# Optimization experiments

Measured on AMD Instinct MI355X. Metric: run time of the kernel, lower is better.

Reference implementation:

```python
import jax, jax.numpy as jnp
import numpy as np

DIM = 1024
INNER = DIM // 2
DSTATE = 8
KSZ = 3
DTRANK = max(INNER // 8, 4)
B, L = 4, 4096


def setup_inputs() -> dict:
    key = jax.random.key(0)
    ks = jax.random.split(key, 8)
    s = 0.02
    x = jax.random.normal(ks[0], (B, L, DIM), dtype=jnp.float32)
    W_in = jax.random.normal(ks[1], (DIM, DIM), dtype=jnp.float32) * s
    Kx = jax.random.normal(ks[2], (INNER, 1, KSZ), dtype=jnp.float32) * 0.1
    Kz = jax.random.normal(ks[3], (INNER, 1, KSZ), dtype=jnp.float32) * 0.1
    W_xproj = jax.random.normal(ks[4], (DTRANK + 2 * DSTATE, INNER), dtype=jnp.float32) * s
    W_dt = jax.random.normal(ks[5], (INNER, DTRANK), dtype=jnp.float32) * s
    # dt bias: inverse_softplus of exp(linspace(log dt_min, log dt_max))
    dt_init = jnp.exp(jnp.linspace(jnp.log(0.02), jnp.log(0.2), INNER))
    b_dt = jnp.log(jnp.expm1(dt_init)).astype(jnp.float32)
    A_log = jnp.log(jnp.tile(jnp.arange(1, DSTATE + 1, dtype=jnp.float32), (INNER, 1)))
    D = jnp.ones((INNER,), dtype=jnp.float32)
    W_out = jax.random.normal(ks[6], (DIM, DIM), dtype=jnp.float32) * s
    return {"x": x, "W_in": W_in, "Kx": Kx, "Kz": Kz, "W_xproj": W_xproj,
            "W_dt": W_dt, "b_dt": b_dt, "A_log": A_log, "D": D, "W_out": W_out}


def _dwconv_silu(u, kern):
    # u: [B,L,C], kern: [C,1,K] depthwise (groups=C), 'same' padding
    c = u.shape[-1]
    v = jnp.transpose(u, (0, 2, 1))  # [B,C,L]
    v = jax.lax.conv_general_dilated(v, kern, (1,), [(KSZ // 2, KSZ // 2)],
                                     dimension_numbers=("NCH", "OIH", "NCH"),
                                     feature_group_count=c)
    return jax.nn.silu(jnp.transpose(v, (0, 2, 1)))


def _forward(x, W_in, Kx, Kz, W_xproj, W_dt, b_dt, A_log, D, W_out):
    h = jnp.einsum("bld,ed->ble", x, W_in)  # Linear(dim,dim), no bias
    xb, zb = jnp.split(h, 2, axis=-1)       # [B,L,INNER] each
    xb = _dwconv_silu(xb, Kx)
    zb = _dwconv_silu(zb, Kz)
    proj = jnp.einsum("blc,oc->blo", xb, W_xproj)
    dt_raw = proj[..., :DTRANK]
    b_raw = proj[..., DTRANK:DTRANK + DSTATE]
    c_raw = proj[..., DTRANK + DSTATE:]
    delta = jnp.clip(jax.nn.softplus(jnp.einsum("blr,cr->blc", dt_raw, W_dt) + b_dt), 1e-4, 1.0)  # [B,L,C]
    b_term = jnp.tanh(b_raw)  # [B,L,N]
    c_term = jnp.tanh(c_raw)  # [B,L,N]
    a = jax.nn.softplus(A_log) + 1e-4  # [C,N]
    decay = jnp.clip(jnp.exp(-delta[..., None] * a), 1e-4, 1.0)        # [B,L,C,N]
    drive = (1.0 - decay) * (b_term[:, :, None, :] * xb[..., None])    # [B,L,C,N]

    def step(state, inp):
        dec_t, drv_t, c_t, x_t = inp  # [B,C,N], [B,C,N], [B,N], [B,C]
        state = dec_t * state + drv_t
        y = jnp.sum(state * c_t[:, None, :], axis=-1) + D * x_t  # [B,C]
        return state, y

    tm = lambda t: jnp.moveaxis(t, 1, 0)  # time-major
    state0 = jnp.zeros((x.shape[0], INNER, DSTATE), dtype=jnp.float32)
    _, ys = jax.lax.scan(step, state0, (tm(decay), tm(drive), tm(c_term), tm(xb)))
    y = jnp.moveaxis(ys, 0, 1)  # [B,L,INNER]
    return jnp.einsum("bld,ed->ble", jnp.concatenate([y, zb], axis=-1), W_out)


def reference(x, W_in, Kx, Kz, W_xproj, W_dt, b_dt, A_log, D, W_out):
    return _forward(x, W_in, Kx, Kz, W_xproj, W_dt, b_dt, A_log, D, W_out)
```

## Files before the change

kernel.cpp:

```cpp
#include <hip/hip_runtime.h>


using bf16x8 = __attribute__((ext_vector_type(8))) short;
using f32x4  = __attribute__((ext_vector_type(4))) float;

__device__ __forceinline__ unsigned short f2bf(float f) {
  unsigned int u = __float_as_uint(f);
  u = u + 0x7fffu + ((u >> 16) & 1u);
  return (unsigned short)(u >> 16);
}

__device__ __forceinline__ float fsoftplus(float x) {
  return (x > 15.f) ? x : __logf(1.f + __expf(x));
}

__device__ __forceinline__ float ftanh(float x) {
  float v = fminf(fmaxf(x, -15.f), 15.f);
  float e = __expf(2.f * v);
  return (e - 1.f) / (e + 1.f);
}

__global__ __launch_bounds__(256) void cvt_bf16_kernel(
    const float* __restrict__ in, unsigned short* __restrict__ out, int n4) {
  int i = blockIdx.x * 256 + threadIdx.x;
  if (i < n4) {
    float4 v = ((const float4*)in)[i];
    ushort4 o;
    o.x = f2bf(v.x); o.y = f2bf(v.y); o.z = f2bf(v.z); o.w = f2bf(v.w);
    ((ushort4*)out)[i] = o;
  }
}

__global__ __launch_bounds__(256) void cvt_wxp_kernel(
    const float* __restrict__ Wx, unsigned short* __restrict__ out) {
  int i = blockIdx.x * 256 + threadIdx.x;
  int row = i >> 9;
  out[i] = (row < 80) ? f2bf(Wx[i]) : (unsigned short)0;
}


__global__ __launch_bounds__(256) void gemm_proj128(
    const unsigned short* __restrict__ A,
    const unsigned short* __restrict__ B,
    unsigned short* __restrict__ dtr, float* __restrict__ bterm,
    float* __restrict__ cterm, int M, int N, int K) {
  __shared__ short As[128 * 32];
  __shared__ short Bs[128 * 32];
  const int m0 = blockIdx.x * 128;
  const int lane = threadIdx.x & 63;
  const int wv = threadIdx.x >> 6;
  const int wm = (wv >> 1) * 64;
  const int wn = (wv & 1) * 64;
  f32x4 acc[4][4] = {};
  const int row_a = wv * 32 + (lane >> 2);
  const int koff = (lane & 3) * 8;
  const unsigned short* gA = A + (size_t)(m0 + row_a) * K + koff;
  const unsigned short* gB = B + (size_t)row_a * K + koff;
  short* lA = &As[(wv * 32) * 32];
  short* lB = &Bs[(wv * 32) * 32];
  const int r = lane & 15;
  const int q = lane >> 4;
  for (int k0 = 0; k0 < K; k0 += 32) {
    __syncthreads();
    __builtin_amdgcn_global_load_lds((const __attribute__((address_space(1))) void*)(const void*)gA,
                                     (__attribute__((address_space(3))) void*)(void*)lA, 16, 0, 0);
    __builtin_amdgcn_global_load_lds((const __attribute__((address_space(1))) void*)(const void*)(gA + 16 * K),
                                     (__attribute__((address_space(3))) void*)(void*)(lA + 16 * 32), 16, 0, 0);
    __builtin_amdgcn_global_load_lds((const __attribute__((address_space(1))) void*)(const void*)gB,
                                     (__attribute__((address_space(3))) void*)(void*)lB, 16, 0, 0);
    __builtin_amdgcn_global_load_lds((const __attribute__((address_space(1))) void*)(const void*)(gB + 16 * K),
                                     (__attribute__((address_space(3))) void*)(void*)(lB + 16 * 32), 16, 0, 0);
    gA += 32; gB += 32;
    __syncthreads();
    bf16x8 av[4], bv[4];
#pragma unroll
    for (int i = 0; i < 4; ++i)
      av[i] = *(const bf16x8*)&As[(wm + i * 16 + r) * 32 + q * 8];
#pragma unroll
    for (int j = 0; j < 4; ++j)
      bv[j] = *(const bf16x8*)&Bs[(wn + j * 16 + r) * 32 + q * 8];
#pragma unroll
    for (int i = 0; i < 4; ++i)
#pragma unroll
      for (int j = 0; j < 4; ++j)
        acc[i][j] = __builtin_amdgcn_mfma_f32_16x16x32_bf16(av[i], bv[j], acc[i][j], 0, 0, 0);
  }
#pragma unroll
  for (int i = 0; i < 4; ++i)
#pragma unroll
    for (int j = 0; j < 4; ++j) {
      const int col = wn + j * 16 + r;
#pragma unroll
      for (int t = 0; t < 4; ++t) {
        const int row = m0 + wm + i * 16 + q * 4 + t;
        float v = acc[i][j][t];
        if (col < 64)      dtr[(size_t)row * 64 + col] = f2bf(v);
        else if (col < 72) bterm[(size_t)row * 8 + (col - 64)] = ftanh(v);
        else if (col < 80) cterm[(size_t)row * 8 + (col - 72)] = ftanh(v);
      }
    }
}

__global__ __launch_bounds__(256) void gemm_dt128(
    const unsigned short* __restrict__ A,
    const unsigned short* __restrict__ B,
    const float* __restrict__ bdt,
    float* __restrict__ C, int M, int N, int K) {
  __shared__ short As[128 * 32];
  __shared__ short Bs[128 * 32];
  const int m0 = blockIdx.x * 128;
  const int n0 = blockIdx.y * 128;
  const int lane = threadIdx.x & 63;
  const int wv = threadIdx.x >> 6;
  const int wm = (wv >> 1) * 64;
  const int wn = (wv & 1) * 64;
  f32x4 acc[4][4] = {};
  const int row_a = wv * 32 + (lane >> 2);
  const int koff = (lane & 3) * 8;
  const unsigned short* gA = A + (size_t)(m0 + row_a) * K + koff;
  const unsigned short* gB = B + (size_t)(n0 + row_a) * K + koff;
  short* lA = &As[(wv * 32) * 32];
  short* lB = &Bs[(wv * 32) * 32];
  const int r = lane & 15;
  const int q = lane >> 4;
  for (int k0 = 0; k0 < K; k0 += 32) {
    __syncthreads();
    __builtin_amdgcn_global_load_lds((const __attribute__((address_space(1))) void*)(const void*)gA,
                                     (__attribute__((address_space(3))) void*)(void*)lA, 16, 0, 0);
    __builtin_amdgcn_global_load_lds((const __attribute__((address_space(1))) void*)(const void*)(gA + 16 * K),
                                     (__attribute__((address_space(3))) void*)(void*)(lA + 16 * 32), 16, 0, 0);
    __builtin_amdgcn_global_load_lds((const __attribute__((address_space(1))) void*)(const void*)gB,
                                     (__attribute__((address_space(3))) void*)(void*)lB, 16, 0, 0);
    __builtin_amdgcn_global_load_lds((const __attribute__((address_space(1))) void*)(const void*)(gB + 16 * K),
                                     (__attribute__((address_space(3))) void*)(void*)(lB + 16 * 32), 16, 0, 0);
    gA += 32; gB += 32;
    __syncthreads();
    bf16x8 av[4], bv[4];
#pragma unroll
    for (int i = 0; i < 4; ++i)
      av[i] = *(const bf16x8*)&As[(wm + i * 16 + r) * 32 + q * 8];
#pragma unroll
    for (int j = 0; j < 4; ++j)
      bv[j] = *(const bf16x8*)&Bs[(wn + j * 16 + r) * 32 + q * 8];
#pragma unroll
    for (int i = 0; i < 4; ++i)
#pragma unroll
      for (int j = 0; j < 4; ++j)
        acc[i][j] = __builtin_amdgcn_mfma_f32_16x16x32_bf16(av[i], bv[j], acc[i][j], 0, 0, 0);
  }
#pragma unroll
  for (int j = 0; j < 4; ++j) {
    const int col = n0 + wn + j * 16 + r;
    const float bb = bdt[col];
#pragma unroll
    for (int i = 0; i < 4; ++i)
#pragma unroll
      for (int t = 0; t < 4; ++t) {
        float v = acc[i][j][t] + bb;
        float delta = fminf(fmaxf(fsoftplus(v), 1e-4f), 1.f);
        C[(size_t)(m0 + wm + i * 16 + q * 4 + t) * N + col] = delta;
      }
  }
}

__device__ __forceinline__ void g256_stage(short* lds, int slot,
    const unsigned short* sp, int ktIdx, int wvLds, int K) {
  const unsigned short* s = sp + ktIdx * 64;
  __builtin_amdgcn_global_load_lds((const __attribute__((address_space(1))) void*)s,
      (__attribute__((address_space(3))) void*)(lds + slot * 8192 + wvLds), 16, 0, 0);
  __builtin_amdgcn_global_load_lds((const __attribute__((address_space(1))) void*)(s + (size_t)64 * K),
      (__attribute__((address_space(3))) void*)(lds + slot * 8192 + 4096 + wvLds), 16, 0, 0);
}

template <int MP, int MH, int NL, int SSLOT, bool VM, int RK, int RP>
__device__ __forceinline__ void g256_phase(
    short* lds, int aSlotOff, int bSlotOff, int aoff, int boff, int wvLds,
    bf16x8 (&av)[4][2], bf16x8 (&bv)[4][2], f32x4 (&acc)[8][4],
    const unsigned short* sp, int ktIdx, int K) {
  g256_stage(lds, SSLOT, sp, ktIdx, wvLds, K);
  if (VM) asm volatile("s_waitcnt vmcnt(6)" ::: "memory");
  __builtin_amdgcn_s_barrier();
  __builtin_amdgcn_s_setprio(1);
#pragma unroll
  for (int ii = 0; ii < 4; ++ii)
#pragma unroll
    for (int jj = 0; jj < 2; ++jj) {
      acc[MH * 4 + ii][NL + jj] = __builtin_amdgcn_mfma_f32_16x16x32_bf16(
          av[ii][0], bv[NL + jj][0], acc[MH * 4 + ii][NL + jj], 0, 0, 0);
      acc[MH * 4 + ii][NL + jj] = __builtin_amdgcn_mfma_f32_16x16x32_bf16(
          av[ii][1], bv[NL + jj][1], acc[MH * 4 + ii][NL + jj], 0, 0, 0);
    }
  __builtin_amdgcn_s_setprio(0);
  if (RK == 2) {
#pragma unroll
    for (int ii = 0; ii < 4; ++ii) {
      av[ii][0] = *(const bf16x8*)&lds[RP * 4 * 8192 + aSlotOff + 4096 + ii * 1024 + aoff];
      av[ii][1] = *(const bf16x8*)&lds[RP * 4 * 8192 + aSlotOff + 4096 + ii * 1024 + (aoff ^ 32)];
    }
  }
  if (RK >= 3) {
#pragma unroll
    for (int ii = 0; ii < 4; ++ii) {
      av[ii][0] = *(const bf16x8*)&lds[RP * 4 * 8192 + aSlotOff + ii * 1024 + aoff];
      av[ii][1] = *(const bf16x8*)&lds[RP * 4 * 8192 + aSlotOff + ii * 1024 + (aoff ^ 32)];
    }
#pragma unroll
    for (int jj = 0; jj < 2; ++jj) {
      bv[jj][0] = *(const bf16x8*)&lds[(RP * 4 + 2) * 8192 + bSlotOff + jj * 1024 + boff];
      bv[jj][1] = *(const bf16x8*)&lds[(RP * 4 + 2) * 8192 + bSlotOff + jj * 1024 + (boff ^ 32)];
    }
  }
  if (RK == 1 || RK == 4) {
#pragma unroll
    for (int jj = 2; jj < 4; ++jj) {
      bv[jj][0] = *(const bf16x8*)&lds[(RP * 4 + 2) * 8192 + bSlotOff + jj * 1024 + boff];
      bv[jj][1] = *(const bf16x8*)&lds[(RP * 4 + 2) * 8192 + bSlotOff + jj * 1024 + (boff ^ 32)];
    }
  }
  __builtin_amdgcn_s_barrier();
}

__global__ __launch_bounds__(512, 2) void gemm256_bt(
    const unsigned short* __restrict__ A,
    const unsigned short* __restrict__ B,
    float* __restrict__ C, int M, int N, int K) {
  __shared__ short lds[8 * 8192];
  const int nmt = M >> 8;
  const int bid = blockIdx.x;
  const int g = nmt >> 3;
  const int xcd = bid & 7;
  const int loc = bid >> 3;
  const int mtile = xcd * g + (loc % g);
  const int ntile = loc / g;
  const int m0 = mtile << 8, n0 = ntile << 8;
  const int tid = threadIdx.x;
  const int w = tid >> 6, lane = tid & 63;
  const int r = lane & 15, q = lane >> 4;
  const int wrow = w >> 2, wcol = w & 3;
  const int srow = tid >> 3;
  const int scol = ((tid & 7) ^ (srow & 7)) << 3;
  const unsigned short* pA0 = A + (size_t)(m0 + srow) * K + scol;
  const unsigned short* pA1 = A + (size_t)(m0 + 128 + srow) * K + scol;
  const unsigned short* pB0 = B + (size_t)(n0 + srow) * K + scol;
  const unsigned short* pB1 = B + (size_t)(n0 + 128 + srow) * K + scol;
  const int wvLds = w * 512;
  const int aSlotOff = wrow * 8192;
  const int bSlotOff = (wcol >> 1) * 8192;
  const int swzc = (q * 8) ^ ((r & 7) << 3);
  const int aoff = r * 64 + swzc;
  const int boff = (wcol & 1) * 4096 + r * 64 + swzc;
  bf16x8 av[4][2], bv[4][2];
  f32x4 acc[8][4] = {};
  const int NT = K >> 6;
  const int NI = NT >> 1;
  g256_stage(lds, 0, pA0, 0, wvLds, K);
  g256_stage(lds, 1, pA1, 0, wvLds, K);
  g256_stage(lds, 2, pB0, 0, wvLds, K);
  g256_stage(lds, 3, pB1, 0, wvLds, K);
  g256_stage(lds, 4, pA0, 1, wvLds, K);
  g256_stage(lds, 6, pB0, 1, wvLds, K);
  g256_stage(lds, 7, pB1, 1, wvLds, K);
  asm volatile("s_waitcnt vmcnt(6)" ::: "memory");
  __builtin_amdgcn_s_barrier();
#pragma unroll
  for (int ii = 0; ii < 4; ++ii) {
    av[ii][0] = *(const bf16x8*)&lds[aSlotOff + ii * 1024 + aoff];
    av[ii][1] = *(const bf16x8*)&lds[aSlotOff + ii * 1024 + (aoff ^ 32)];
  }
#pragma unroll
  for (int jj = 0; jj < 2; ++jj) {
    bv[jj][0] = *(const bf16x8*)&lds[2 * 8192 + bSlotOff + jj * 1024 + boff];
    bv[jj][1] = *(const bf16x8*)&lds[2 * 8192 + bSlotOff + jj * 1024 + (boff ^ 32)];
  }
#pragma unroll 1
  for (int it = 0; it < NI; ++it) {
    const int ktO = 2 * it + 1;
    const int kt2 = (2 * it + 2 < NT) ? 2 * it + 2 : NT - 1;
    const int kt3 = (2 * it + 3 < NT) ? 2 * it + 3 : NT - 1;
    g256_phase<0,0,0, 5, false, 1, 0>(lds, aSlotOff, bSlotOff, aoff, boff, wvLds, av, bv, acc, pA1, ktO, K);
    g256_phase<0,0,2, 2, false, 2, 0>(lds, aSlotOff, bSlotOff, aoff, boff, wvLds, av, bv, acc, pB0, kt2, K);
    g256_phase<0,1,2, 3, false, 0, 0>(lds, aSlotOff, bSlotOff, aoff, boff, wvLds, av, bv, acc, pB1, kt2, K);
    g256_phase<0,1,0, 0, true,  4, 1>(lds, aSlotOff, bSlotOff, aoff, boff, wvLds, av, bv, acc, pA0, kt2, K);
    g256_phase<1,0,0, 1, false, 0, 0>(lds, aSlotOff, bSlotOff, aoff, boff, wvLds, av, bv, acc, pA1, kt2, K);
    g256_phase<1,0,2, 6, false, 2, 1>(lds, aSlotOff, bSlotOff, aoff, boff, wvLds, av, bv, acc, pB0, kt3, K);
    g256_phase<1,1,2, 7, false, 0, 0>(lds, aSlotOff, bSlotOff, aoff, boff, wvLds, av, bv, acc, pB1, kt3, K);
    g256_phase<1,1,0, 4, true,  3, 0>(lds, aSlotOff, bSlotOff, aoff, boff, wvLds, av, bv, acc, pA0, kt3, K);
  }
  asm volatile("s_waitcnt vmcnt(0) lgkmcnt(0)" ::: "memory");
  float* Cw = C + (size_t)(m0 + wrow * 128) * N + n0 + wcol * 64;
#pragma unroll
  for (int ii = 0; ii < 8; ++ii)
#pragma unroll
    for (int jj = 0; jj < 4; ++jj)
#pragma unroll
      for (int t = 0; t < 4; ++t)
        Cw[(size_t)(ii * 16 + q * 4 + t) * N + jj * 16 + r] = acc[ii][jj][t];
}

__global__ __launch_bounds__(256) void conv_silu_v4(
    const float* __restrict__ h, const float* __restrict__ Kx, const float* __restrict__ Kz,
    float* __restrict__ xb, unsigned short* __restrict__ xbbf,
    unsigned short* __restrict__ cat) {
  int tid = blockIdx.x * 256 + threadIdx.x;
  int c4 = (tid & 255) << 2;
  int bl = tid >> 8;
  int l = bl & 4095;
  const float* Kp; int c;
  if (c4 < 512) { Kp = Kx; c = c4; } else { Kp = Kz; c = c4 - 512; }
  const float4* K4 = (const float4*)(Kp + c * 3);
  float4 ka = K4[0], kb = K4[1], kc = K4[2];
  size_t idx = (size_t)bl * 1024 + c4;
  float4 zero = make_float4(0.f, 0.f, 0.f, 0.f);
  float4 um = (l > 0)    ? *(const float4*)(h + idx - 1024) : zero;
  float4 u0 = *(const float4*)(h + idx);
  float4 up = (l < 4095) ? *(const float4*)(h + idx + 1024) : zero;
  float v0 = um.x * ka.x + u0.x * ka.y + up.x * ka.z;
  float v1 = um.y * ka.w + u0.y * kb.x + up.y * kb.y;
  float v2 = um.z * kb.z + u0.z * kb.w + up.z * kc.x;
  float v3 = um.w * kc.y + u0.w * kc.z + up.w * kc.w;
  float o0 = v0 / (1.f + __expf(-v0));
  float o1 = v1 / (1.f + __expf(-v1));
  float o2 = v2 / (1.f + __expf(-v2));
  float o3 = v3 / (1.f + __expf(-v3));
  ushort4 ob;
  ob.x = f2bf(o0); ob.y = f2bf(o1); ob.z = f2bf(o2); ob.w = f2bf(o3);
  if (c4 < 512) {
    size_t xo = (size_t)bl * 512 + c4;
    *(float4*)(xb + xo) = make_float4(o0, o1, o2, o3);
    *(ushort4*)(xbbf + xo) = ob;
  } else {
    *(ushort4*)(cat + idx) = ob;
  }
}

__global__ __launch_bounds__(256) void scan_p1(
    const float* __restrict__ delta_in, const float* __restrict__ bterm,
    const float* __restrict__ xb, const float* __restrict__ A_log,
    float* __restrict__ Aprod, float* __restrict__ Bpart) {
  int tid = threadIdx.x;
  int gid = blockIdx.x;
  int chunk = gid & 127, half = (gid >> 7) & 1, b = gid >> 8;
  int c = half * 256 + tid;
  float4 a0 = *(const float4*)&A_log[c * 8];
  float4 a1 = *(const float4*)&A_log[c * 8 + 4];
  float na[8] = {a0.x, a0.y, a0.z, a0.w, a1.x, a1.y, a1.z, a1.w};
#pragma unroll
  for (int s = 0; s < 8; ++s) na[s] = -(fsoftplus(na[s]) + 1e-4f);
  int l0 = chunk * 32;
  size_t base  = ((size_t)b * 4096 + l0) * 512 + c;
  size_t bbase = ((size_t)b * 4096 + l0) * 8;
  float S[8] = {}, Ap[8] = {1.f, 1.f, 1.f, 1.f, 1.f, 1.f, 1.f, 1.f};
  for (int i = 0; i < 32; ++i) {
    float delta = delta_in[base];
    float xv = xb[base];
    float4 bt0 = *(const float4*)&bterm[bbase];
    float4 bt1 = *(const float4*)&bterm[bbase + 4];
    float bt[8] = {bt0.x, bt0.y, bt0.z, bt0.w, bt1.x, bt1.y, bt1.z, bt1.w};
#pragma unroll
    for (int s = 0; s < 8; ++s) {
      float dec = fminf(fmaxf(__expf(delta * na[s]), 1e-4f), 1.f);
      float btx = bt[s] * xv;
      S[s] = dec * S[s] + (btx - dec * btx);
      Ap[s] *= dec;
    }
    base += 512; bbase += 8;
  }
  size_t o = (size_t)chunk * 16384 + ((size_t)(b * 512 + c)) * 8;
  *(float4*)&Aprod[o]     = make_float4(Ap[0], Ap[1], Ap[2], Ap[3]);
  *(float4*)&Aprod[o + 4] = make_float4(Ap[4], Ap[5], Ap[6], Ap[7]);
  *(float4*)&Bpart[o]     = make_float4(S[0], S[1], S[2], S[3]);
  *(float4*)&Bpart[o + 4] = make_float4(S[4], S[5], S[6], S[7]);
}

__global__ __launch_bounds__(256) void scan_p2(
    const float* __restrict__ Aprod, const float* __restrict__ Bpart,
    float* __restrict__ initst) {
  int t = blockIdx.x * 256 + threadIdx.x;
  float st = 0.f;
  for (int cb = 0; cb < 128; cb += 8) {
    float a[8], bb[8];
#pragma unroll
    for (int j = 0; j < 8; ++j) {
      size_t o = (size_t)(cb + j) * 16384 + t;
      a[j] = Aprod[o]; bb[j] = Bpart[o];
    }
#pragma unroll
    for (int j = 0; j < 8; ++j) {
      size_t o = (size_t)(cb + j) * 16384 + t;
      initst[o] = st;
      st = a[j] * st + bb[j];
    }
  }
}

__global__ __launch_bounds__(256) void scan_p3(
    const float* __restrict__ delta_in, const float* __restrict__ bterm,
    const float* __restrict__ cterm, const float* __restrict__ xb,
    const float* __restrict__ A_log, const float* __restrict__ Dp,
    const float* __restrict__ initst, unsigned short* __restrict__ cat) {
  int tid = threadIdx.x;
  int gid = blockIdx.x;
  int chunk = gid & 127, half = (gid >> 7) & 1, b = gid >> 8;
  int c = half * 256 + tid;
  float4 a0 = *(const float4*)&A_log[c * 8];
  float4 a1 = *(const float4*)&A_log[c * 8 + 4];
  float na[8] = {a0.x, a0.y, a0.z, a0.w, a1.x, a1.y, a1.z, a1.w};
#pragma unroll
  for (int s = 0; s < 8; ++s) na[s] = -(fsoftplus(na[s]) + 1e-4f);
  float Dv = Dp[c];
  size_t o = (size_t)chunk * 16384 + ((size_t)(b * 512 + c)) * 8;
  float4 s0 = *(const float4*)&initst[o];
  float4 s1 = *(const float4*)&initst[o + 4];
  float S[8] = {s0.x, s0.y, s0.z, s0.w, s1.x, s1.y, s1.z, s1.w};
  int l0 = chunk * 32;
  size_t base  = ((size_t)b * 4096 + l0) * 512 + c;
  size_t bbase = ((size_t)b * 4096 + l0) * 8;
  size_t cbase = ((size_t)b * 4096 + l0) * 1024 + c;
  for (int i = 0; i < 32; ++i) {
    float delta = delta_in[base];
    float xv = xb[base];
    float4 bt0 = *(const float4*)&bterm[bbase];
    float4 bt1 = *(const float4*)&bterm[bbase + 4];
    float4 ct0 = *(const float4*)&cterm[bbase];
    float4 ct1 = *(const float4*)&cterm[bbase + 4];
    float bt[8] = {bt0.x, bt0.y, bt0.z, bt0.w, bt1.x, bt1.y, bt1.z, bt1.w};
    float ct[8] = {ct0.x, ct0.y, ct0.z, ct0.w, ct1.x, ct1.y, ct1.z, ct1.w};
    float acc = Dv * xv;
#pragma unroll
    for (int s = 0; s < 8; ++s) {
      float dec = fminf(fmaxf(__expf(delta * na[s]), 1e-4f), 1.f);
      float btx = bt[s] * xv;
      S[s] = dec * S[s] + (btx - dec * btx);
      acc += S[s] * ct[s];
    }
    cat[cbase] = f2bf(acc);
    base += 512; bbase += 8; cbase += 1024;
  }
}

extern "C" void kernel_launch(void* const* d_in, const int* in_sizes, int n_in,
                              void* d_out, int out_size, void* d_ws, size_t ws_size,
                              hipStream_t stream) {
  (void)in_sizes; (void)n_in; (void)out_size; (void)ws_size;
  const float* x       = (const float*)d_in[0];
  const float* W_in    = (const float*)d_in[1];
  const float* Kx      = (const float*)d_in[2];
  const float* Kz      = (const float*)d_in[3];
  const float* W_xproj = (const float*)d_in[4];
  const float* W_dt    = (const float*)d_in[5];
  const float* b_dt    = (const float*)d_in[6];
  const float* A_log   = (const float*)d_in[7];
  const float* Dp      = (const float*)d_in[8];
  const float* W_out   = (const float*)d_in[9];
  float* out = (float*)d_out;

  char* w = (char*)d_ws;
  unsigned short* xbf  = (unsigned short*)(w);
  float* xb    = (float*)(w + 33554432);
  float* draw  = (float*)(w + 67108864);
  float* bterm = (float*)(w + 100663296);
  float* cterm = (float*)(w + 101187584);
  float* Aprod = (float*)(w + 101711872);
  float* Bpart = (float*)(w + 110100480);
  float* initst = (float*)(w + 118489088);
  unsigned short* winbf  = (unsigned short*)(w + 126877696);
  unsigned short* woutbf = (unsigned short*)(w + 128974848);
  unsigned short* dtr    = (unsigned short*)(w + 131072000);
  unsigned short* wxp_bf = (unsigned short*)(w + 133169152);
  unsigned short* wd_bf  = (unsigned short*)(w + 133300224);
  unsigned short* xbbf = (unsigned short*)Aprod;
  float* h = out;

  cvt_bf16_kernel<<<16384, 256, 0, stream>>>(x, xbf, 4194304);
  cvt_bf16_kernel<<<1024, 256, 0, stream>>>(W_in, winbf, 262144);
  cvt_bf16_kernel<<<1024, 256, 0, stream>>>(W_out, woutbf, 262144);
  cvt_bf16_kernel<<<32, 256, 0, stream>>>(W_dt, wd_bf, 8192);
  cvt_wxp_kernel<<<256, 256, 0, stream>>>(W_xproj, wxp_bf);

  gemm256_bt<<<256, 512, 0, stream>>>(xbf, winbf, h, 16384, 1024, 1024);

  conv_silu_v4<<<16384, 256, 0, stream>>>(h, Kx, Kz, xb, xbbf, xbf );

  gemm_proj128<<<128, 256, 0, stream>>>(xbbf, wxp_bf, dtr, bterm, cterm, 16384, 128, 512);
  gemm_dt128<<<dim3(128, 4), 256, 0, stream>>>(dtr, wd_bf, b_dt, draw, 16384, 512, 64);

  scan_p1<<<1024, 256, 0, stream>>>(draw, bterm, xb, A_log, Aprod, Bpart);
  scan_p2<<<64, 256, 0, stream>>>(Aprod, Bpart, initst);
  scan_p3<<<1024, 256, 0, stream>>>(draw, bterm, cterm, xb, A_log, Dp, initst, xbf );

  gemm256_bt<<<256, 512, 0, stream>>>(xbf, woutbf, out, 16384, 1024, 1024);
}
```

Measured before the change: 338.9 us.

## Fuse conversion kernels, rework GEMM LDS prefetch schedule, roll conv over sequence

Merges the five fp32-to-bf16 conversion launches into one kernel to cut launch overhead. Restructures the 256x256 GEMM phase schedule so LDS fragment reads happen at the start of each phase, before the barrier, with adjusted vmcnt/lgkmcnt waits and a changed staging order. Rewrites the depthwise conv+SiLU so each thread walks 16 consecutive positions, reusing neighbour rows in registers instead of reloading three rows per output. The GEMM reschedule is the riskiest part, since it changes the slot-to-tile mapping and the wait counts.

After: 318.4 us. 6.1% less time.

```diff
diff --git a/kernel.cpp b/kernel.cpp
--- a/kernel.cpp
+++ b/kernel.cpp
@@ -20,22 +20,31 @@
   return (e - 1.f) / (e + 1.f);
 }
 
-__global__ __launch_bounds__(256) void cvt_bf16_kernel(
-    const float* __restrict__ in, unsigned short* __restrict__ out, int n4) {
-  int i = blockIdx.x * 256 + threadIdx.x;
-  if (i < n4) {
-    float4 v = ((const float4*)in)[i];
-    ushort4 o;
-    o.x = f2bf(v.x); o.y = f2bf(v.y); o.z = f2bf(v.z); o.w = f2bf(v.w);
-    ((ushort4*)out)[i] = o;
-  }
-}
-
-__global__ __launch_bounds__(256) void cvt_wxp_kernel(
-    const float* __restrict__ Wx, unsigned short* __restrict__ out) {
-  int i = blockIdx.x * 256 + threadIdx.x;
-  int row = i >> 9;
-  out[i] = (row < 80) ? f2bf(Wx[i]) : (unsigned short)0;
+__device__ __forceinline__ void cvt4(const float* __restrict__ in,
+                                     unsigned short* __restrict__ out, int i) {
+  float4 v = ((const float4*)in)[i];
+  ushort4 o;
+  o.x = f2bf(v.x); o.y = f2bf(v.y); o.z = f2bf(v.z); o.w = f2bf(v.w);
+  ((ushort4*)out)[i] = o;
+}
+
+__global__ __launch_bounds__(256) void prep_all(
+    const float* __restrict__ x, const float* __restrict__ Win,
+    const float* __restrict__ Wout, const float* __restrict__ Wdt,
+    const float* __restrict__ Wxp,
+    unsigned short* __restrict__ xbf, unsigned short* __restrict__ winbf,
+    unsigned short* __restrict__ woutbf, unsigned short* __restrict__ wdbf,
+    unsigned short* __restrict__ wxpbf) {
+  int b = blockIdx.x, t = threadIdx.x;
+  if (b < 16384)      cvt4(x,    xbf,    b * 256 + t);
+  else if (b < 17408) cvt4(Win,  winbf,  (b - 16384) * 256 + t);
+  else if (b < 18432) cvt4(Wout, woutbf, (b - 17408) * 256 + t);
+  else if (b < 18464) cvt4(Wdt,  wdbf,   (b - 18432) * 256 + t);
+  else {
+    int i = (b - 18464) * 256 + t;
+    int row = i >> 9;
+    wxpbf[i] = (row < 80) ? f2bf(Wxp[i]) : (unsigned short)0;
+  }
 }
 
 
@@ -172,51 +181,41 @@
       (__attribute__((address_space(3))) void*)(lds + slot * 8192 + 4096 + wvLds), 16, 0, 0);
 }
 
-template <int MP, int MH, int NL, int SSLOT, bool VM, int RK, int RP>
+template <int PAR, int MH, int NHLO, bool RA, bool RB, int SSLOT, bool VM, bool HINT>
 __device__ __forceinline__ void g256_phase(
     short* lds, int aSlotOff, int bSlotOff, int aoff, int boff, int wvLds,
     bf16x8 (&av)[4][2], bf16x8 (&bv)[4][2], f32x4 (&acc)[8][4],
     const unsigned short* sp, int ktIdx, int K) {
+  if (RA) {
+#pragma unroll
+    for (int ii = 0; ii < 4; ++ii) {
+      av[ii][0] = *(const bf16x8*)&lds[PAR * 4 * 8192 + aSlotOff + MH * 4096 + ii * 1024 + aoff];
+      av[ii][1] = *(const bf16x8*)&lds[PAR * 4 * 8192 + aSlotOff + MH * 4096 + ii * 1024 + (aoff ^ 32)];
+    }
+  }
+  if (RB) {
+#pragma unroll
+    for (int jj = 0; jj < 2; ++jj) {
+      bv[NHLO + jj][0] = *(const bf16x8*)&lds[(PAR * 4 + 2) * 8192 + bSlotOff + (NHLO + jj) * 1024 + boff];
+      bv[NHLO + jj][1] = *(const bf16x8*)&lds[(PAR * 4 + 2) * 8192 + bSlotOff + (NHLO + jj) * 1024 + (boff ^ 32)];
+    }
+  }
   g256_stage(lds, SSLOT, sp, ktIdx, wvLds, K);
-  if (VM) asm volatile("s_waitcnt vmcnt(6)" ::: "memory");
+  if (HINT) asm volatile("s_waitcnt lgkmcnt(8)");
+  if (VM) asm volatile("s_waitcnt vmcnt(4)" ::: "memory");
   __builtin_amdgcn_s_barrier();
+  asm volatile("s_waitcnt lgkmcnt(0)" ::: "memory");
   __builtin_amdgcn_s_setprio(1);
 #pragma unroll
   for (int ii = 0; ii < 4; ++ii)
 #pragma unroll
     for (int jj = 0; jj < 2; ++jj) {
-      acc[MH * 4 + ii][NL + jj] = __builtin_amdgcn_mfma_f32_16x16x32_bf16(
-          av[ii][0], bv[NL + jj][0], acc[MH * 4 + ii][NL + jj], 0, 0, 0);
-      acc[MH * 4 + ii][NL + jj] = __builtin_amdgcn_mfma_f32_16x16x32_bf16(
-          av[ii][1], bv[NL + jj][1], acc[MH * 4 + ii][NL + jj], 0, 0, 0);
+      acc[MH * 4 + ii][NHLO + jj] = __builtin_amdgcn_mfma_f32_16x16x32_bf16(
+          av[ii][0], bv[NHLO + jj][0], acc[MH * 4 + ii][NHLO + jj], 0, 0, 0);
+      acc[MH * 4 + ii][NHLO + jj] = __builtin_amdgcn_mfma_f32_16x16x32_bf16(
+          av[ii][1], bv[NHLO + jj][1], acc[MH * 4 + ii][NHLO + jj], 0, 0, 0);
     }
   __builtin_amdgcn_s_setprio(0);
-  if (RK == 2) {
-#pragma unroll
-    for (int ii = 0; ii < 4; ++ii) {
-      av[ii][0] = *(const bf16x8*)&lds[RP * 4 * 8192 + aSlotOff + 4096 + ii * 1024 + aoff];
-      av[ii][1] = *(const bf16x8*)&lds[RP * 4 * 8192 + aSlotOff + 4096 + ii * 1024 + (aoff ^ 32)];
-    }
-  }
-  if (RK >= 3) {
-#pragma unroll
-    for (int ii = 0; ii < 4; ++ii) {
-      av[ii][0] = *(const bf16x8*)&lds[RP * 4 * 8192 + aSlotOff + ii * 1024 + aoff];
-      av[ii][1] = *(const bf16x8*)&lds[RP * 4 * 8192 + aSlotOff + ii * 1024 + (aoff ^ 32)];
-    }
-#pragma unroll
-    for (int jj = 0; jj < 2; ++jj) {
-      bv[jj][0] = *(const bf16x8*)&lds[(RP * 4 + 2) * 8192 + bSlotOff + jj * 1024 + boff];
-      bv[jj][1] = *(const bf16x8*)&lds[(RP * 4 + 2) * 8192 + bSlotOff + jj * 1024 + (boff ^ 32)];
-    }
-  }
-  if (RK == 1 || RK == 4) {
-#pragma unroll
-    for (int jj = 2; jj < 4; ++jj) {
-      bv[jj][0] = *(const bf16x8*)&lds[(RP * 4 + 2) * 8192 + bSlotOff + jj * 1024 + boff];
-      bv[jj][1] = *(const bf16x8*)&lds[(RP * 4 + 2) * 8192 + bSlotOff + jj * 1024 + (boff ^ 32)];
-    }
-  }
   __builtin_amdgcn_s_barrier();
 }
 
@@ -257,34 +256,23 @@
   g256_stage(lds, 1, pA1, 0, wvLds, K);
   g256_stage(lds, 2, pB0, 0, wvLds, K);
   g256_stage(lds, 3, pB1, 0, wvLds, K);
-  g256_stage(lds, 4, pA0, 1, wvLds, K);
   g256_stage(lds, 6, pB0, 1, wvLds, K);
   g256_stage(lds, 7, pB1, 1, wvLds, K);
-  asm volatile("s_waitcnt vmcnt(6)" ::: "memory");
+  asm volatile("s_waitcnt vmcnt(4)" ::: "memory");
   __builtin_amdgcn_s_barrier();
-#pragma unroll
-  for (int ii = 0; ii < 4; ++ii) {
-    av[ii][0] = *(const bf16x8*)&lds[aSlotOff + ii * 1024 + aoff];
-    av[ii][1] = *(const bf16x8*)&lds[aSlotOff + ii * 1024 + (aoff ^ 32)];
-  }
-#pragma unroll
-  for (int jj = 0; jj < 2; ++jj) {
-    bv[jj][0] = *(const bf16x8*)&lds[2 * 8192 + bSlotOff + jj * 1024 + boff];
-    bv[jj][1] = *(const bf16x8*)&lds[2 * 8192 + bSlotOff + jj * 1024 + (boff ^ 32)];
-  }
 #pragma unroll 1
   for (int it = 0; it < NI; ++it) {
-    const int ktO = 2 * it + 1;
-    const int kt2 = (2 * it + 2 < NT) ? 2 * it + 2 : NT - 1;
-    const int kt3 = (2 * it + 3 < NT) ? 2 * it + 3 : NT - 1;
-    g256_phase<0,0,0, 5, false, 1, 0>(lds, aSlotOff, bSlotOff, aoff, boff, wvLds, av, bv, acc, pA1, ktO, K);
-    g256_phase<0,0,2, 2, false, 2, 0>(lds, aSlotOff, bSlotOff, aoff, boff, wvLds, av, bv, acc, pB0, kt2, K);
-    g256_phase<0,1,2, 3, false, 0, 0>(lds, aSlotOff, bSlotOff, aoff, boff, wvLds, av, bv, acc, pB1, kt2, K);
-    g256_phase<0,1,0, 0, true,  4, 1>(lds, aSlotOff, bSlotOff, aoff, boff, wvLds, av, bv, acc, pA0, kt2, K);
-    g256_phase<1,0,0, 1, false, 0, 0>(lds, aSlotOff, bSlotOff, aoff, boff, wvLds, av, bv, acc, pA1, kt2, K);
-    g256_phase<1,0,2, 6, false, 2, 1>(lds, aSlotOff, bSlotOff, aoff, boff, wvLds, av, bv, acc, pB0, kt3, K);
-    g256_phase<1,1,2, 7, false, 0, 0>(lds, aSlotOff, bSlotOff, aoff, boff, wvLds, av, bv, acc, pB1, kt3, K);
-    g256_phase<1,1,0, 4, true,  3, 0>(lds, aSlotOff, bSlotOff, aoff, boff, wvLds, av, bv, acc, pA0, kt3, K);
+    const int ktO  = 2 * it + 1;
+    const int ktE2 = (2 * it + 2 < NT) ? 2 * it + 2 : NT - 1;
+    const int ktO2 = (2 * it + 3 < NT) ? 2 * it + 3 : NT - 1;
+    g256_phase<0, 0, 0, true,  true,  4, false, true >(lds, aSlotOff, bSlotOff, aoff, boff, wvLds, av, bv, acc, pA0, ktO,  K);
+    g256_phase<0, 0, 2, false, true,  5, false, false>(lds, aSlotOff, bSlotOff, aoff, boff, wvLds, av, bv, acc, pA1, ktO,  K);
+    g256_phase<0, 1, 2, true,  false, 2, false, false>(lds, aSlotOff, bSlotOff, aoff, boff, wvLds, av, bv, acc, pB0, ktE2, K);
+    g256_phase<0, 1, 0, false, false, 0, true,  false>(lds, aSlotOff, bSlotOff, aoff, boff, wvLds, av, bv, acc, pA0, ktE2, K);
+    g256_phase<1, 0, 0, true,  true,  1, false, true >(lds, aSlotOff, bSlotOff, aoff, boff, wvLds, av, bv, acc, pA1, ktE2, K);
+    g256_phase<1, 0, 2, false, true,  3, false, false>(lds, aSlotOff, bSlotOff, aoff, boff, wvLds, av, bv, acc, pB1, ktE2, K);
+    g256_phase<1, 1, 2, true,  false, 6, false, false>(lds, aSlotOff, bSlotOff, aoff, boff, wvLds, av, bv, acc, pB0, ktO2, K);
+    g256_phase<1, 1, 0, false, false, 7, true,  false>(lds, aSlotOff, bSlotOff, aoff, boff, wvLds, av, bv, acc, pB1, ktO2, K);
   }
   asm volatile("s_waitcnt vmcnt(0) lgkmcnt(0)" ::: "memory");
   float* Cw = C + (size_t)(m0 + wrow * 128) * N + n0 + wcol * 64;
@@ -297,39 +285,45 @@
         Cw[(size_t)(ii * 16 + q * 4 + t) * N + jj * 16 + r] = acc[ii][jj][t];
 }
 
-__global__ __launch_bounds__(256) void conv_silu_v4(
+__global__ __launch_bounds__(256) void conv_silu_roll(
     const float* __restrict__ h, const float* __restrict__ Kx, const float* __restrict__ Kz,
     float* __restrict__ xb, unsigned short* __restrict__ xbbf,
     unsigned short* __restrict__ cat) {
-  int tid = blockIdx.x * 256 + threadIdx.x;
-  int c4 = (tid & 255) << 2;
-  int bl = tid >> 8;
-  int l = bl & 4095;
+  const int c4 = threadIdx.x << 2;
+  const int bt = blockIdx.x >> 8;
+  const int lt = blockIdx.x & 255;
+  const int l0 = lt << 4;
   const float* Kp; int c;
   if (c4 < 512) { Kp = Kx; c = c4; } else { Kp = Kz; c = c4 - 512; }
   const float4* K4 = (const float4*)(Kp + c * 3);
-  float4 ka = K4[0], kb = K4[1], kc = K4[2];
-  size_t idx = (size_t)bl * 1024 + c4;
-  float4 zero = make_float4(0.f, 0.f, 0.f, 0.f);
-  float4 um = (l > 0)    ? *(const float4*)(h + idx - 1024) : zero;
-  float4 u0 = *(const float4*)(h + idx);
-  float4 up = (l < 4095) ? *(const float4*)(h + idx + 1024) : zero;
-  float v0 = um.x * ka.x + u0.x * ka.y + up.x * ka.z;
-  float v1 = um.y * ka.w + u0.y * kb.x + up.y * kb.y;
-  float v2 = um.z * kb.z + u0.z * kb.w + up.z * kc.x;
-  float v3 = um.w * kc.y + u0.w * kc.z + up.w * kc.w;
-  float o0 = v0 / (1.f + __expf(-v0));
-  float o1 = v1 / (1.f + __expf(-v1));
-  float o2 = v2 / (1.f + __expf(-v2));
-  float o3 = v3 / (1.f + __expf(-v3));
-  ushort4 ob;
-  ob.x = f2bf(o0); ob.y = f2bf(o1); ob.z = f2bf(o2); ob.w = f2bf(o3);
-  if (c4 < 512) {
-    size_t xo = (size_t)bl * 512 + c4;
-    *(float4*)(xb + xo) = make_float4(o0, o1, o2, o3);
-    *(ushort4*)(xbbf + xo) = ob;
-  } else {
-    *(ushort4*)(cat + idx) = ob;
+  const float4 ka = K4[0], kb = K4[1], kc = K4[2];
+  size_t rowbase = ((size_t)bt * 4096 + l0) * 1024 + c4;
+  size_t xrow    = ((size_t)bt * 4096 + l0) * 512 + c4;
+  const float4 zero = make_float4(0.f, 0.f, 0.f, 0.f);
+  float4 um = (l0 > 0) ? *(const float4*)(h + rowbase - 1024) : zero;
+  float4 u0 = *(const float4*)(h + rowbase);
+#pragma unroll 4
+  for (int s = 0; s < 16; ++s) {
+    const int l = l0 + s;
+    float4 up = (l < 4095) ? *(const float4*)(h + rowbase + 1024) : zero;
+    float v0 = um.x * ka.x + u0.x * ka.y + up.x * ka.z;
+    float v1 = um.y * ka.w + u0.y * kb.x + up.y * kb.y;
+    float v2 = um.z * kb.z + u0.z * kb.w + up.z * kc.x;
+    float v3 = um.w * kc.y + u0.w * kc.z + up.w * kc.w;
+    float o0 = v0 / (1.f + __expf(-v0));
+    float o1 = v1 / (1.f + __expf(-v1));
+    float o2 = v2 / (1.f + __expf(-v2));
+    float o3 = v3 / (1.f + __expf(-v3));
+    ushort4 ob;
+    ob.x = f2bf(o0); ob.y = f2bf(o1); ob.z = f2bf(o2); ob.w = f2bf(o3);
+    if (c4 < 512) {
+      *(float4*)(xb + xrow) = make_float4(o0, o1, o2, o3);
+      *(ushort4*)(xbbf + xrow) = ob;
+    } else {
+      *(ushort4*)(cat + rowbase) = ob;
+    }
+    um = u0; u0 = up;
+    rowbase += 1024; xrow += 512;
   }
 }
 
@@ -471,15 +465,12 @@
   unsigned short* xbbf = (unsigned short*)Aprod;
   float* h = out;
 
-  cvt_bf16_kernel<<<16384, 256, 0, stream>>>(x, xbf, 4194304);
-  cvt_bf16_kernel<<<1024, 256, 0, stream>>>(W_in, winbf, 262144);
-  cvt_bf16_kernel<<<1024, 256, 0, stream>>>(W_out, woutbf, 262144);
-  cvt_bf16_kernel<<<32, 256, 0, stream>>>(W_dt, wd_bf, 8192);
-  cvt_wxp_kernel<<<256, 256, 0, stream>>>(W_xproj, wxp_bf);
+  prep_all<<<18720, 256, 0, stream>>>(x, W_in, W_out, W_dt, W_xproj,
+                                      xbf, winbf, woutbf, wd_bf, wxp_bf);
 
   gemm256_bt<<<256, 512, 0, stream>>>(xbf, winbf, h, 16384, 1024, 1024);
 
-  conv_silu_v4<<<16384, 256, 0, stream>>>(h, Kx, Kz, xb, xbbf, xbf );
+  conv_silu_roll<<<1024, 256, 0, stream>>>(h, Kx, Kz, xb, xbbf, xbf );
 
   gemm_proj128<<<128, 256, 0, stream>>>(xbbf, wxp_bf, dtr, bterm, cterm, 16384, 128, 512);
   gemm_dt128<<<dim3(128, 4), 256, 0, stream>>>(dtr, wd_bf, b_dt, draw, 16384, 512, 64);
```
